# Kernel tuning notes

Hardware: AMD Instinct MI355X
Metric: run time of the kernel (lower is better)

Reference implementation:

```python
import jax, jax.numpy as jnp
import numpy as np

B, G, IN, F, O = 65536, 6, 512, 256, 18


def setup_inputs() -> dict:
    key = jax.random.key(0)
    ks = jax.random.split(key, 9)
    return {
        "state": jax.random.normal(ks[0], (B, IN), dtype=jnp.float32),
        "action": jax.random.randint(ks[1], (B, 1), 0, O, dtype=jnp.int64),
        "idx": jax.random.randint(ks[2], (B,), 0, G, dtype=jnp.int64),
        # per-game expert Linear weights (stored [in, out] so fwd is x @ W)
        "W1": jax.random.normal(ks[3], (G, IN, F), dtype=jnp.float32) * (1.0 / np.sqrt(IN)),
        "b1": jnp.zeros((G, F), dtype=jnp.float32),
        # shared layer
        "W2": jax.random.normal(ks[4], (F, F), dtype=jnp.float32) * (1.0 / np.sqrt(F)),
        "b2": jnp.zeros((F,), dtype=jnp.float32),
        # per-game Q heads
        "Wq": jax.random.normal(ks[5], (G, F, O), dtype=jnp.float32) * (1.0 / np.sqrt(F)),
        "bq": jnp.zeros((G, O), dtype=jnp.float32),
    }


def reference(state, action, idx, W1, b1, W2, b2, Wq, bq):
    # The torch code processes samples grouped by np.unique(idx) and then
    # torch.cat's the groups: this is a stable sort of samples by idx value.
    perm = jnp.argsort(idx)  # jnp.argsort is stable by default
    sp = state[perm]         # [B, IN], samples in group-sorted order
    ip = idx[perm]           # [B]

    # per-game expert: compute all G tiny linears, select the routed one
    h_all = jax.nn.sigmoid(jnp.einsum('bi,gif->bgf', sp, W1) + b1)  # [B,G,F]
    h1 = jnp.take_along_axis(h_all, ip[:, None, None], axis=1)[:, 0, :]  # [B,F]

    # shared layer ('relu' branch)
    h_f = jax.nn.relu(h1 @ W2 + b2)  # [B,F]

    # stacked per-game heads
    q = jnp.tanh(jnp.einsum('bf,gfo->bgo', h_f, Wq) + bq)  # [B,G,O]

    # action gather: q_acted[b,g] = q[b,g,action[b,0]] (action in ORIGINAL order,
    # exactly as in the torch code, which gathers on the permuted-row q)
    a = jnp.broadcast_to(action[:, :1], (B, G))[..., None]  # [B,G,1]
    q_acted = jnp.take_along_axis(q, a, axis=2)[..., 0]     # [B,G]

    # idx gather (again with idx in ORIGINAL order, matching the torch code)
    q_out = jnp.take_along_axis(q_acted, idx[:, None], axis=1)[:, 0]  # [B]
    return q_out
```

## Files before the change

### kernel.cpp

```cpp
#include <hip/hip_runtime.h>
#include <math.h>

#define B_N 65536
#define G_N 6
#define IN_N 512
#define F_N 256
#define O_N 18

#define NB 256
#define CHUNK 256

#define TBM 32
#define MAXT (B_N / TBM + G_N)

typedef __bf16 bf16x8 __attribute__((ext_vector_type(8)));
typedef float f32x4 __attribute__((ext_vector_type(4)));

#define WS_BC     0
#define WS_BOFF   8192
#define WS_NTILES 16448
#define WS_DESC   16512
#define WS_W1F    65536
#define WS_W2F    (WS_W1F + 1572864)
#define WS_WQT    (WS_W2F + 131072)
#define WS_PERM   4194304

__device__ __forceinline__ unsigned short f2bf(float f) {
    union { float f; unsigned u; } a; a.f = f;
    unsigned r = a.u + 0x7fffu + ((a.u >> 16) & 1u);
    return (unsigned short)(r >> 16);
}
__device__ __forceinline__ unsigned pack2(float a, float b) {
    return (unsigned)f2bf(a) | ((unsigned)f2bf(b) << 16);
}
__device__ __forceinline__ bf16x8 asbf(uint4 u) {
    union { uint4 u; bf16x8 b; } c; c.u = u; return c.b;
}

__global__ void k_hist(const int* __restrict__ idx, int* __restrict__ bc) {
    __shared__ int cnt[G_N];
    int t = threadIdx.x;
    if (t < G_N) cnt[t] = 0;
    __syncthreads();
    int e = blockIdx.x * CHUNK + t;
    atomicAdd(&cnt[idx[e]], 1);
    __syncthreads();
    if (t < G_N) bc[blockIdx.x * G_N + t] = cnt[t];
}

__global__ void k_prefix(const int* __restrict__ bc, int* __restrict__ boff,
                         int* __restrict__ ntiles, int* __restrict__ desc) {
    __shared__ int sbc[NB * G_N];
    __shared__ int tot[G_N], st[G_N];
    __shared__ int tstart[G_N + 1];
    int t = threadIdx.x;
    for (int i = t; i < NB * G_N; i += 256) sbc[i] = bc[i];
    __syncthreads();
    int w = t >> 6, l = t & 63;
    for (int g = w; g < G_N; g += 4) {
        int v[4]; int s = 0;
#pragma unroll
        for (int j = 0; j < 4; j++) { v[j] = sbc[(l * 4 + j) * G_N + g]; s += v[j]; }
        int inc = s;
#pragma unroll
        for (int o = 1; o < 64; o <<= 1) { int x = __shfl_up(inc, o, 64); if (l >= o) inc += x; }
        int run = inc - s;
        if (l == 63) tot[g] = inc;
#pragma unroll
        for (int j = 0; j < 4; j++) { sbc[(l * 4 + j) * G_N + g] = run; run += v[j]; }
    }
    __syncthreads();
    if (t == 0) {
        int acc = 0;
        for (int g = 0; g < G_N; g++) { st[g] = acc; acc += tot[g]; }
        int nt = 0;
        for (int g = 0; g < G_N; g++) { tstart[g] = nt; nt += (tot[g] + TBM - 1) / TBM; }
        tstart[G_N] = nt;
        *ntiles = nt;
    }
    __syncthreads();
    for (int i = t; i < NB * G_N; i += 256) boff[i] = sbc[i] + st[i % G_N];
    int nt = tstart[G_N];
    for (int i = t; i < MAXT; i += 256) {
        int gd = 0, r0 = 0, nr = 0;
        if (i < nt) {
            int g = 0;
            while (g < G_N - 1 && i >= tstart[g + 1]) g++;
            int k = i - tstart[g];
            r0 = st[g] + k * TBM;
            int rem = tot[g] - k * TBM;
            nr = rem < TBM ? rem : TBM;
            gd = g;
        }
        desc[i * 3 + 0] = gd; desc[i * 3 + 1] = r0; desc[i * 3 + 2] = nr;
    }
}

__global__ void k_scatter(const int* __restrict__ idx, const int* __restrict__ boff,
                          int* __restrict__ perm) {
    __shared__ int wcnt[4][G_N];
    __shared__ int base[G_N];
    int t = threadIdx.x, w = t >> 6, l = t & 63;
    int e = blockIdx.x * CHUNK + t;
    int g = idx[e];
    int rank = 0;
    for (int gg = 0; gg < G_N; gg++) {
        unsigned long long m = __ballot(g == gg);
        if (g == gg) rank = __popcll(m & ((1ull << l) - 1ull));
        if (l == 0) wcnt[w][gg] = __popcll(m);
    }
    if (t < G_N) base[t] = boff[blockIdx.x * G_N + t];
    __syncthreads();
    int off = base[g] + rank;
    for (int ww = 0; ww < w; ww++) off += wcnt[ww][g];
    perm[off] = e;
}

__global__ void k_pack_all(const float* __restrict__ W1, const float* __restrict__ W2,
                           const float* __restrict__ Wq,
                           unsigned short* __restrict__ W1f, unsigned short* __restrict__ W2f,
                           float* __restrict__ WqT) {
    int kf = blockIdx.x, w = blockIdx.y, z = blockIdx.z;
    if (z == 6 && kf >= 8) {
        int tid = ((kf - 8) * 8 + w) * 128 + threadIdx.x;
        for (int e = tid; e < G_N * O_N * F_N; e += 8192) {
            int f = e & (F_N - 1);
            int go = e >> 8;
            int g = go / O_N, o = go - g * O_N;
            WqT[e] = Wq[((long)g * F_N + f) * O_N + o];
        }
        return;
    }
    const float* src;
    unsigned short* dst;
    int kfTot;
    if (z < 6) { src = W1 + (long)z * IN_N * F_N; dst = W1f + (long)z * IN_N * F_N; kfTot = 16; }
    else       { src = W2; dst = W2f; kfTot = 8; }
    int f = threadIdx.x >> 6, l = threadIdx.x & 63;
    int lrow = l & 15, q = l >> 4;
    int n = w * 32 + f * 16 + lrow;
    int k0 = kf * 32 + q * 8;
    const float* s = src + (long)k0 * F_N + n;
    unsigned o[4];
#pragma unroll
    for (int j = 0; j < 4; j++)
        o[j] = pack2(s[(2 * j) * F_N], s[(2 * j + 1) * F_N]);
    unsigned short* d = dst + ((((long)w * kfTot + kf) * 2 + f) * 64 + l) * 8;
    uint4 v = { o[0], o[1], o[2], o[3] };
    *(uint4*)d = v;
}

__global__ __launch_bounds__(512, 6) void k_fused(
    const float* __restrict__ state, const char* __restrict__ w1f,
    const char* __restrict__ w2f, const float* __restrict__ wqt,
    const float* __restrict__ b1, const float* __restrict__ b2,
    const float* __restrict__ bqv,
    const int* __restrict__ action, const int* __restrict__ idx,
    const int* __restrict__ perm, const int* __restrict__ desc,
    float* __restrict__ out) {
    int td = blockIdx.x;
    int g = desc[td * 3 + 0], row0 = desc[td * 3 + 1], nr = desc[td * 3 + 2];
    if (nr == 0) return;

    __shared__ __align__(16) unsigned short smA[TBM * 512];
    __shared__ float partial[TBM][9];
    __shared__ int gq[TBM], actv[TBM];
    unsigned short* smH = smA;

    int t = threadIdx.x, w = t >> 6, l = t & 63;
    int lrow = l & 15, q = l >> 4;
    int x0 = lrow & 7;

    const char* B1 = w1f + (((long)g * 8 + w) << 15) + l * 16;
    uint4 nb0 = *(const uint4*)(B1);
    uint4 nb1 = *(const uint4*)(B1 + 1024);

    if (t < TBM) {
        int pos = row0 + t; if (pos > B_N - 1) pos = B_N - 1;
        gq[t] = idx[pos];
        actv[t] = action[pos];
    }

    {
        int m = t >> 4, s = t & 15;
        int pr = row0 + m; if (pr > B_N - 1) pr = B_N - 1;
        const float* src = state + (long)perm[pr] * IN_N + s * 4;
        int cb = s >> 1, h = s & 1, mx = m & 7;
        char* rowbase = (char*)smA + m * 1024 + h * 8;
#pragma unroll
        for (int j = 0; j < 8; j++) {
            float4 v = *(const float4*)(src + j * 64);
            uint2 p = { pack2(v.x, v.y), pack2(v.z, v.w) };
            int c = (cb + j * 8) ^ mx;
            *(uint2*)(rowbase + c * 16) = p;
        }
    }
    __syncthreads();

    const char* ar[2];
#pragma unroll
    for (int i = 0; i < 2; i++) ar[i] = (const char*)smA + (i * 16 + lrow) * 1024;

    f32x4 acc[2][2];
#pragma unroll
    for (int i = 0; i < 2; i++)
#pragma unroll
        for (int j = 0; j < 2; j++) acc[i][j] = (f32x4){0.f, 0.f, 0.f, 0.f};

#pragma unroll
    for (int kf = 0; kf < 16; kf++) {
        uint4 cb0 = nb0, cb1 = nb1;
        if (kf < 15) {
            nb0 = *(const uint4*)(B1 + (kf + 1) * 2048);
            nb1 = *(const uint4*)(B1 + (kf + 1) * 2048 + 1024);
        }
        int c = ((kf * 4 + q) ^ x0) * 16;
        bf16x8 af[2];
#pragma unroll
        for (int i = 0; i < 2; i++) af[i] = *(const bf16x8*)(ar[i] + c);
        bf16x8 b0 = asbf(cb0), b1v = asbf(cb1);
#pragma unroll
        for (int i = 0; i < 2; i++) {
            acc[i][0] = __builtin_amdgcn_mfma_f32_16x16x32_bf16(af[i], b0, acc[i][0], 0, 0, 0);
            acc[i][1] = __builtin_amdgcn_mfma_f32_16x16x32_bf16(af[i], b1v, acc[i][1], 0, 0, 0);
        }
    }
    __syncthreads();

    {
        int col0 = w * 32 + lrow;
#pragma unroll
        for (int j = 0; j < 2; j++) {
            int col = col0 + j * 16;
            float bias = b1[g * F_N + col];
            int cc = col >> 3, cb2 = (col & 7) * 2;
#pragma unroll
            for (int i = 0; i < 2; i++)
#pragma unroll
                for (int r = 0; r < 4; r++) {
                    int row = i * 16 + q * 4 + r;
                    float v = acc[i][j][r] + bias;
                    float sg = 1.0f / (1.0f + __expf(-v));
                    int c = cc ^ (row & 7);
                    *(unsigned short*)((char*)smH + row * 512 + c * 16 + cb2) = f2bf(sg);
                }
        }
    }
    __syncthreads();

    const char* B2 = w2f + ((long)w << 14) + l * 16;
    const char* hr[2];
#pragma unroll
    for (int i = 0; i < 2; i++) hr[i] = (const char*)smH + (i * 16 + lrow) * 512;

    f32x4 acc2[2][2];
#pragma unroll
    for (int i = 0; i < 2; i++)
#pragma unroll
        for (int j = 0; j < 2; j++) acc2[i][j] = (f32x4){0.f, 0.f, 0.f, 0.f};

    uint4 m0 = *(const uint4*)(B2);
    uint4 m1 = *(const uint4*)(B2 + 1024);
#pragma unroll
    for (int kf = 0; kf < 8; kf++) {
        uint4 c0 = m0, c1 = m1;
        if (kf < 7) {
            m0 = *(const uint4*)(B2 + (kf + 1) * 2048);
            m1 = *(const uint4*)(B2 + (kf + 1) * 2048 + 1024);
        }
        int c = ((kf * 4 + q) ^ x0) * 16;
        bf16x8 af[2];
#pragma unroll
        for (int i = 0; i < 2; i++) af[i] = *(const bf16x8*)(hr[i] + c);
        bf16x8 b0 = asbf(c0), b1v = asbf(c1);
#pragma unroll
        for (int i = 0; i < 2; i++) {
            acc2[i][0] = __builtin_amdgcn_mfma_f32_16x16x32_bf16(af[i], b0, acc2[i][0], 0, 0, 0);
            acc2[i][1] = __builtin_amdgcn_mfma_f32_16x16x32_bf16(af[i], b1v, acc2[i][1], 0, 0, 0);
        }
    }

    {
        int col0 = w * 32 + lrow;
        float bias0 = b2[col0], bias1 = b2[col0 + 16];
#pragma unroll
        for (int i = 0; i < 2; i++)
#pragma unroll
            for (int r = 0; r < 4; r++) {
                int row = i * 16 + q * 4 + r;
                const float* wp = wqt + ((long)gq[row] * O_N + actv[row]) * F_N;
                float v0 = fmaxf(acc2[i][0][r] + bias0, 0.0f);
                float v1 = fmaxf(acc2[i][1][r] + bias1, 0.0f);
                float s = v0 * wp[col0] + v1 * wp[col0 + 16];
                s += __shfl_xor(s, 1, 64);
                s += __shfl_xor(s, 2, 64);
                s += __shfl_xor(s, 4, 64);
                s += __shfl_xor(s, 8, 64);
                if (lrow == 0) partial[row][w] = s;
            }
    }
    __syncthreads();
    if (t < TBM && t < nr) {
        float s = 0.f;
#pragma unroll
        for (int ww = 0; ww < 8; ww++) s += partial[t][ww];
        out[row0 + t] = tanhf(s + bqv[gq[t] * O_N + actv[t]]);
    }
}

extern "C" void kernel_launch(void* const* d_in, const int* in_sizes, int n_in,
                              void* d_out, int out_size, void* d_ws, size_t ws_size,
                              hipStream_t stream) {
    const float* state  = (const float*)d_in[0];
    const int*   action = (const int*)d_in[1];
    const int*   idx    = (const int*)d_in[2];
    const float* W1     = (const float*)d_in[3];
    const float* b1     = (const float*)d_in[4];
    const float* W2     = (const float*)d_in[5];
    const float* b2     = (const float*)d_in[6];
    const float* Wq     = (const float*)d_in[7];
    const float* bq     = (const float*)d_in[8];
    float* out = (float*)d_out;

    char* ws = (char*)d_ws;
    int* bc      = (int*)(ws + WS_BC);
    int* boff    = (int*)(ws + WS_BOFF);
    int* ntiles  = (int*)(ws + WS_NTILES);
    int* desc    = (int*)(ws + WS_DESC);
    unsigned short* W1f = (unsigned short*)(ws + WS_W1F);
    unsigned short* W2f = (unsigned short*)(ws + WS_W2F);
    float* WqT   = (float*)(ws + WS_WQT);
    int* perm    = (int*)(ws + WS_PERM);

    k_hist<<<NB, CHUNK, 0, stream>>>(idx, bc);
    k_prefix<<<1, 256, 0, stream>>>(bc, boff, ntiles, desc);
    k_scatter<<<NB, CHUNK, 0, stream>>>(idx, boff, perm);
    k_pack_all<<<dim3(16, 8, 7), 128, 0, stream>>>(W1, W2, Wq, W1f, W2f, WqT);
    k_fused<<<MAXT, 512, 0, stream>>>(state, (const char*)W1f, (const char*)W2f, WqT,
                                      b1, b2, bq, action, idx, perm, desc, out);
}
```

Measured before the change: 252.2 us.

## Double row tile to 64 and stage state input in two K halves

Raises the per-block row tile from 32 to 64 so each W1/W2 fragment fetched from global memory feeds twice as many MFMAs. To hold shared memory at the same size, the state tile is loaded and converted to bf16 in two 256-column halves, each followed by its own MFMA pass, with an extra sync between them. The launch-bounds occupancy hint rises to 8 blocks, and each thread now carries twice the accumulators, which risks register pressure and spills. Tail tiles per group also get larger, so more padded rows are computed.

```diff
diff --git a/kernel.cpp b/kernel.cpp
--- a/kernel.cpp
+++ b/kernel.cpp
@@ -10,7 +10,7 @@
 #define NB 256
 #define CHUNK 256
 
-#define TBM 32
+#define TBM 64
 #define MAXT (B_N / TBM + G_N)
 
 typedef __bf16 bf16x8 __attribute__((ext_vector_type(8)));
@@ -150,7 +150,7 @@
     *(uint4*)d = v;
 }
 
-__global__ __launch_bounds__(512, 6) void k_fused(
+__global__ __launch_bounds__(512, 8) void k_fused(
     const float* __restrict__ state, const char* __restrict__ w1f,
     const char* __restrict__ w2f, const float* __restrict__ wqt,
     const float* __restrict__ b1, const float* __restrict__ b2,
@@ -162,7 +162,7 @@
     int g = desc[td * 3 + 0], row0 = desc[td * 3 + 1], nr = desc[td * 3 + 2];
     if (nr == 0) return;
 
-    __shared__ __align__(16) unsigned short smA[TBM * 512];
+    __shared__ __align__(16) unsigned short smA[TBM * 256];
     __shared__ float partial[TBM][9];
     __shared__ int gq[TBM], actv[TBM];
     unsigned short* smH = smA;
@@ -181,46 +181,73 @@
         actv[t] = action[pos];
     }
 
-    {
-        int m = t >> 4, s = t & 15;
-        int pr = row0 + m; if (pr > B_N - 1) pr = B_N - 1;
-        const float* src = state + (long)perm[pr] * IN_N + s * 4;
-        int cb = s >> 1, h = s & 1, mx = m & 7;
-        char* rowbase = (char*)smA + m * 1024 + h * 8;
-#pragma unroll
-        for (int j = 0; j < 8; j++) {
-            float4 v = *(const float4*)(src + j * 64);
-            uint2 p = { pack2(v.x, v.y), pack2(v.z, v.w) };
-            int c = (cb + j * 8) ^ mx;
-            *(uint2*)(rowbase + c * 16) = p;
-        }
-    }
-    __syncthreads();
-
-    const char* ar[2];
-#pragma unroll
-    for (int i = 0; i < 2; i++) ar[i] = (const char*)smA + (i * 16 + lrow) * 1024;
-
-    f32x4 acc[2][2];
-#pragma unroll
-    for (int i = 0; i < 2; i++)
+    int sm = t >> 3, ss = t & 7;
+    int spr = row0 + sm; if (spr > B_N - 1) spr = B_N - 1;
+    const float* srow = state + (long)perm[spr] * IN_N + ss * 4;
+    int scb = ss >> 1, smx = sm & 7;
+    char* srb = (char*)smA + sm * 512 + (ss & 1) * 8;
+
+#pragma unroll
+    for (int j = 0; j < 8; j++) {
+        float4 v = *(const float4*)(srow + j * 32);
+        uint2 pk = { pack2(v.x, v.y), pack2(v.z, v.w) };
+        int c = (scb + j * 4) ^ smx;
+        *(uint2*)(srb + c * 16) = pk;
+    }
+    __syncthreads();
+
+    const char* ar[4];
+#pragma unroll
+    for (int i = 0; i < 4; i++) ar[i] = (const char*)smA + (i * 16 + lrow) * 512;
+
+    f32x4 acc[4][2];
+#pragma unroll
+    for (int i = 0; i < 4; i++)
 #pragma unroll
         for (int j = 0; j < 2; j++) acc[i][j] = (f32x4){0.f, 0.f, 0.f, 0.f};
 
 #pragma unroll
-    for (int kf = 0; kf < 16; kf++) {
+    for (int kfl = 0; kfl < 8; kfl++) {
+        uint4 cb0 = nb0, cb1 = nb1;
+        nb0 = *(const uint4*)(B1 + (kfl + 1) * 2048);
+        nb1 = *(const uint4*)(B1 + (kfl + 1) * 2048 + 1024);
+        int c = ((kfl * 4 + q) ^ x0) * 16;
+        bf16x8 af[4];
+#pragma unroll
+        for (int i = 0; i < 4; i++) af[i] = *(const bf16x8*)(ar[i] + c);
+        bf16x8 b0 = asbf(cb0), b1v = asbf(cb1);
+#pragma unroll
+        for (int i = 0; i < 4; i++) {
+            acc[i][0] = __builtin_amdgcn_mfma_f32_16x16x32_bf16(af[i], b0, acc[i][0], 0, 0, 0);
+            acc[i][1] = __builtin_amdgcn_mfma_f32_16x16x32_bf16(af[i], b1v, acc[i][1], 0, 0, 0);
+        }
+    }
+    __syncthreads();
+
+#pragma unroll
+    for (int j = 0; j < 8; j++) {
+        float4 v = *(const float4*)(srow + 256 + j * 32);
+        uint2 pk = { pack2(v.x, v.y), pack2(v.z, v.w) };
+        int c = (scb + j * 4) ^ smx;
+        *(uint2*)(srb + c * 16) = pk;
+    }
+    __syncthreads();
+
+#pragma unroll
+    for (int kfl = 0; kfl < 8; kfl++) {
+        int kf = 8 + kfl;
         uint4 cb0 = nb0, cb1 = nb1;
         if (kf < 15) {
             nb0 = *(const uint4*)(B1 + (kf + 1) * 2048);
             nb1 = *(const uint4*)(B1 + (kf + 1) * 2048 + 1024);
         }
-        int c = ((kf * 4 + q) ^ x0) * 16;
-        bf16x8 af[2];
-#pragma unroll
-        for (int i = 0; i < 2; i++) af[i] = *(const bf16x8*)(ar[i] + c);
+        int c = ((kfl * 4 + q) ^ x0) * 16;
+        bf16x8 af[4];
+#pragma unroll
+        for (int i = 0; i < 4; i++) af[i] = *(const bf16x8*)(ar[i] + c);
         bf16x8 b0 = asbf(cb0), b1v = asbf(cb1);
 #pragma unroll
-        for (int i = 0; i < 2; i++) {
+        for (int i = 0; i < 4; i++) {
             acc[i][0] = __builtin_amdgcn_mfma_f32_16x16x32_bf16(af[i], b0, acc[i][0], 0, 0, 0);
             acc[i][1] = __builtin_amdgcn_mfma_f32_16x16x32_bf16(af[i], b1v, acc[i][1], 0, 0, 0);
         }
@@ -235,7 +262,7 @@
             float bias = b1[g * F_N + col];
             int cc = col >> 3, cb2 = (col & 7) * 2;
 #pragma unroll
-            for (int i = 0; i < 2; i++)
+            for (int i = 0; i < 4; i++)
 #pragma unroll
                 for (int r = 0; r < 4; r++) {
                     int row = i * 16 + q * 4 + r;
@@ -249,13 +276,13 @@
     __syncthreads();
 
     const char* B2 = w2f + ((long)w << 14) + l * 16;
-    const char* hr[2];
-#pragma unroll
-    for (int i = 0; i < 2; i++) hr[i] = (const char*)smH + (i * 16 + lrow) * 512;
-
-    f32x4 acc2[2][2];
-#pragma unroll
-    for (int i = 0; i < 2; i++)
+    const char* hr[4];
+#pragma unroll
+    for (int i = 0; i < 4; i++) hr[i] = (const char*)smH + (i * 16 + lrow) * 512;
+
+    f32x4 acc2[4][2];
+#pragma unroll
+    for (int i = 0; i < 4; i++)
 #pragma unroll
         for (int j = 0; j < 2; j++) acc2[i][j] = (f32x4){0.f, 0.f, 0.f, 0.f};
 
@@ -269,12 +296,12 @@
             m1 = *(const uint4*)(B2 + (kf + 1) * 2048 + 1024);
         }
         int c = ((kf * 4 + q) ^ x0) * 16;
-        bf16x8 af[2];
-#pragma unroll
-        for (int i = 0; i < 2; i++) af[i] = *(const bf16x8*)(hr[i] + c);
+        bf16x8 af[4];
+#pragma unroll
+        for (int i = 0; i < 4; i++) af[i] = *(const bf16x8*)(hr[i] + c);
         bf16x8 b0 = asbf(c0), b1v = asbf(c1);
 #pragma unroll
-        for (int i = 0; i < 2; i++) {
+        for (int i = 0; i < 4; i++) {
             acc2[i][0] = __builtin_amdgcn_mfma_f32_16x16x32_bf16(af[i], b0, acc2[i][0], 0, 0, 0);
             acc2[i][1] = __builtin_amdgcn_mfma_f32_16x16x32_bf16(af[i], b1v, acc2[i][1], 0, 0, 0);
         }
@@ -284,7 +311,7 @@
         int col0 = w * 32 + lrow;
         float bias0 = b2[col0], bias1 = b2[col0 + 16];
 #pragma unroll
-        for (int i = 0; i < 2; i++)
+        for (int i = 0; i < 4; i++)
 #pragma unroll
             for (int r = 0; r < 4; r++) {
                 int row = i * 16 + q * 4 + r;
```

Measured after the change: 448.2 us. 1.78x slower.

## Remap blocks to XCDs and double-depth prefetch of weight fragments

Applied to the files above, without the earlier changes.

Block IDs are remapped so that consecutive tile descriptors land on the same XCD, giving same-group tiles L2 locality for the W1 expert weights. The register prefetch of W1 and W2 fragments goes from one step ahead to two steps ahead. The perm load is also hoisted ahead of the other setup loads. This costs extra registers, which may reduce occupancy under launch_bounds(512,6), and the hardcoded 257/256 split assumes MAXT=2054.

```diff
diff --git a/kernel.cpp b/kernel.cpp
--- a/kernel.cpp
+++ b/kernel.cpp
@@ -158,7 +158,10 @@
     const int* __restrict__ action, const int* __restrict__ idx,
     const int* __restrict__ perm, const int* __restrict__ desc,
     float* __restrict__ out) {
-    int td = blockIdx.x;
+    int bid = blockIdx.x;
+    int xcd = bid & 7, jj = bid >> 3;
+    int td = (xcd < 6 ? xcd * 257 : 6 * 257 + (xcd - 6) * 256) + jj;
+
     int g = desc[td * 3 + 0], row0 = desc[td * 3 + 1], nr = desc[td * 3 + 2];
     if (nr == 0) return;
 
@@ -172,8 +175,14 @@
     int x0 = lrow & 7;
 
     const char* B1 = w1f + (((long)g * 8 + w) << 15) + l * 16;
-    uint4 nb0 = *(const uint4*)(B1);
-    uint4 nb1 = *(const uint4*)(B1 + 1024);
+    uint4 p00 = *(const uint4*)(B1);
+    uint4 p01 = *(const uint4*)(B1 + 1024);
+    uint4 p10 = *(const uint4*)(B1 + 2048);
+    uint4 p11 = *(const uint4*)(B1 + 2048 + 1024);
+
+    int m = t >> 4, s = t & 15;
+    int pr = row0 + m; if (pr > B_N - 1) pr = B_N - 1;
+    int prow = perm[pr];
 
     if (t < TBM) {
         int pos = row0 + t; if (pos > B_N - 1) pos = B_N - 1;
@@ -182,9 +191,7 @@
     }
 
     {
-        int m = t >> 4, s = t & 15;
-        int pr = row0 + m; if (pr > B_N - 1) pr = B_N - 1;
-        const float* src = state + (long)perm[pr] * IN_N + s * 4;
+        const float* src = state + (long)prow * IN_N + s * 4;
         int cb = s >> 1, h = s & 1, mx = m & 7;
         char* rowbase = (char*)smA + m * 1024 + h * 8;
 #pragma unroll
@@ -209,10 +216,16 @@
 
 #pragma unroll
     for (int kf = 0; kf < 16; kf++) {
-        uint4 cb0 = nb0, cb1 = nb1;
-        if (kf < 15) {
-            nb0 = *(const uint4*)(B1 + (kf + 1) * 2048);
-            nb1 = *(const uint4*)(B1 + (kf + 1) * 2048 + 1024);
+        uint4 cb0 = (kf & 1) ? p10 : p00;
+        uint4 cb1 = (kf & 1) ? p11 : p01;
+        if (kf < 14) {
+            if (kf & 1) {
+                p10 = *(const uint4*)(B1 + (kf + 2) * 2048);
+                p11 = *(const uint4*)(B1 + (kf + 2) * 2048 + 1024);
+            } else {
+                p00 = *(const uint4*)(B1 + (kf + 2) * 2048);
+                p01 = *(const uint4*)(B1 + (kf + 2) * 2048 + 1024);
+            }
         }
         int c = ((kf * 4 + q) ^ x0) * 16;
         bf16x8 af[2];
@@ -259,14 +272,22 @@
 #pragma unroll
         for (int j = 0; j < 2; j++) acc2[i][j] = (f32x4){0.f, 0.f, 0.f, 0.f};
 
-    uint4 m0 = *(const uint4*)(B2);
-    uint4 m1 = *(const uint4*)(B2 + 1024);
+    uint4 q00 = *(const uint4*)(B2);
+    uint4 q01 = *(const uint4*)(B2 + 1024);
+    uint4 q10 = *(const uint4*)(B2 + 2048);
+    uint4 q11 = *(const uint4*)(B2 + 2048 + 1024);
 #pragma unroll
     for (int kf = 0; kf < 8; kf++) {
-        uint4 c0 = m0, c1 = m1;
-        if (kf < 7) {
-            m0 = *(const uint4*)(B2 + (kf + 1) * 2048);
-            m1 = *(const uint4*)(B2 + (kf + 1) * 2048 + 1024);
+        uint4 c0 = (kf & 1) ? q10 : q00;
+        uint4 c1 = (kf & 1) ? q11 : q01;
+        if (kf < 6) {
+            if (kf & 1) {
+                q10 = *(const uint4*)(B2 + (kf + 2) * 2048);
+                q11 = *(const uint4*)(B2 + (kf + 2) * 2048 + 1024);
+            } else {
+                q00 = *(const uint4*)(B2 + (kf + 2) * 2048);
+                q01 = *(const uint4*)(B2 + (kf + 2) * 2048 + 1024);
+            }
         }
         int c = ((kf * 4 + q) ^ x0) * 16;
         bf16x8 af[2];
@@ -291,20 +312,20 @@
                 const float* wp = wqt + ((long)gq[row] * O_N + actv[row]) * F_N;
                 float v0 = fmaxf(acc2[i][0][r] + bias0, 0.0f);
                 float v1 = fmaxf(acc2[i][1][r] + bias1, 0.0f);
-                float s = v0 * wp[col0] + v1 * wp[col0 + 16];
-                s += __shfl_xor(s, 1, 64);
-                s += __shfl_xor(s, 2, 64);
-                s += __shfl_xor(s, 4, 64);
-                s += __shfl_xor(s, 8, 64);
-                if (lrow == 0) partial[row][w] = s;
+                float s2 = v0 * wp[col0] + v1 * wp[col0 + 16];
+                s2 += __shfl_xor(s2, 1, 64);
+                s2 += __shfl_xor(s2, 2, 64);
+                s2 += __shfl_xor(s2, 4, 64);
+                s2 += __shfl_xor(s2, 8, 64);
+                if (lrow == 0) partial[row][w] = s2;
             }
     }
     __syncthreads();
     if (t < TBM && t < nr) {
-        float s = 0.f;
-#pragma unroll
-        for (int ww = 0; ww < 8; ww++) s += partial[t][ww];
-        out[row0 + t] = tanhf(s + bqv[gq[t] * O_N + actv[t]]);
+        float s2 = 0.f;
+#pragma unroll
+        for (int ww = 0; ww < 8; ww++) s2 += partial[t][ww];
+        out[row0 + t] = tanhf(s2 + bqv[gq[t] * O_N + actv[t]]);
     }
 }
 
```

Result: no change. 253.2 us (+0.4%).
